# Kernel optimization log

Hardware: AMD Instinct MI355X
Metric: run time of the kernel (lower is better)

## Reference

```python
import jax, jax.numpy as jnp
import numpy as np

B, L, E, H = 4, 2048, 1024, 16
D = E // H
RBF_GAMMA = 0.5


def setup_inputs() -> dict:
    key = jax.random.key(0)
    ks = jax.random.split(key, 8)
    s = 1.0 / np.sqrt(E)  # linear init scale
    return {
        "query": jax.random.normal(ks[0], (B, L, E), jnp.float32),
        "key": jax.random.normal(ks[1], (B, L, E), jnp.float32),
        "value": jax.random.normal(ks[2], (B, L, E), jnp.float32),
        "Wq": jax.random.normal(ks[3], (E, E), jnp.float32) * s,
        "bq": jnp.zeros((E,), jnp.float32),
        "Wk": jax.random.normal(ks[4], (E, E), jnp.float32) * s,
        "bk": jnp.zeros((E,), jnp.float32),
        "Wv": jax.random.normal(ks[5], (E, E), jnp.float32) * s,
        "bv": jnp.zeros((E,), jnp.float32),
        "Wo": jax.random.normal(ks[6], (E, E), jnp.float32) * s,
        "bo": jnp.zeros((E,), jnp.float32),
    }


def _heads(x):
    # (B, L, E) -> (B, H, L, D)
    b, l, _ = x.shape
    return x.reshape(b, l, H, D).transpose(0, 2, 1, 3)


def _rbf_scores(q, k):
    # score[b,h,i,j] = -gamma * ||q_i - k_j||^2   (log of RBF kernel)
    q2 = jnp.sum(q * q, axis=-1)  # (B,H,Lq)
    k2 = jnp.sum(k * k, axis=-1)  # (B,H,Lk)
    qk = jnp.einsum("bhqd,bhkd->bhqk", q, k)  # (B,H,Lq,Lk)
    sqd = q2[..., :, None] + k2[..., None, :] - 2.0 * qk
    return -RBF_GAMMA * sqd


def reference(query, key, value, Wq, bq, Wk, bk, Wv, bv, Wo, bo):
    # Linear projections (torch nn.Linear: x @ W.T + b)
    q = _heads(query @ Wq.T + bq)
    k = _heads(key @ Wk.T + bk)
    v = _heads(value @ Wv.T + bv)
    scores = _rbf_scores(q, k)            # (B,H,L,L)
    attn = jax.nn.softmax(scores, axis=-1)  # dropout p=0.0 (eval)
    out = jnp.einsum("bhqk,bhkd->bhqd", attn, v)
    out = out.transpose(0, 2, 1, 3).reshape(B, L, E)  # merge heads
    return out @ Wo.T + bo
```

## Files before the change

### kernel.cpp

```cpp
#include <hip/hip_runtime.h>
#include <hip/hip_bf16.h>
#include <stdint.h>

#define DEV __device__ __forceinline__

typedef __attribute__((ext_vector_type(8))) __bf16 bf16x8;
typedef __attribute__((ext_vector_type(4))) float f32x4;
typedef __attribute__((ext_vector_type(16))) float f32x16;
typedef __attribute__((ext_vector_type(2))) unsigned int u32x2;
typedef __attribute__((ext_vector_type(4))) unsigned int u32x4;

#define LOG2E 1.44269504088896f

DEV unsigned short f2bf(float f) {
    union { float f; unsigned int u; } v; v.f = f;
    unsigned int u = v.u;
    return (unsigned short)((u + 0x7FFFu + ((u >> 16) & 1u)) >> 16);
}
DEV float bf2f(unsigned short s) {
    union { unsigned int u; float f; } v; v.u = ((unsigned int)s) << 16;
    return v.f;
}

DEV f32x4 mfma16(bf16x8 a, bf16x8 b, f32x4 c) {
    return __builtin_amdgcn_mfma_f32_16x16x32_bf16(a, b, c, 0, 0, 0);
}
DEV f32x16 mfma32(bf16x8 a, bf16x8 b, f32x16 c) {
    return __builtin_amdgcn_mfma_f32_32x32x16_bf16(a, b, c, 0, 0, 0);
}
DEV float exp2a(float x) { float r; asm("v_exp_f32 %0, %1" : "=v"(r) : "v"(x)); return r; }
DEV unsigned cvtpk(float lo, float hi) {
    unsigned r; asm("v_cvt_pk_bf16_f32 %0, %1, %2" : "=v"(r) : "v"(lo), "v"(hi)); return r;
}
DEV void plswap(unsigned& x, unsigned& y) {
    asm volatile("v_permlane32_swap_b32 %0, %1" : "+v"(x), "+v"(y));
}

#define GLOAD_LDS16(g, l)                                                          \
    __builtin_amdgcn_global_load_lds((__attribute__((address_space(1))) void*)(g), \
                                     (__attribute__((address_space(3))) void*)(l), \
                                     16, 0, 0)

#define VMCNT(N) asm volatile("s_waitcnt vmcnt(" #N ")" ::: "memory")
#define LGKM0    asm volatile("s_waitcnt lgkmcnt(0)" ::: "memory")
#define RBAR()   do { __builtin_amdgcn_s_barrier(); __builtin_amdgcn_sched_barrier(0); } while (0)

__global__ void k_cvtw(const float* __restrict__ i0, const float* __restrict__ i1,
                       const float* __restrict__ i2, const float* __restrict__ i3,
                       unsigned short* __restrict__ o0, unsigned short* __restrict__ o1,
                       unsigned short* __restrict__ o2, unsigned short* __restrict__ o3) {
    int z = blockIdx.y;
    const float* in = z == 0 ? i0 : (z == 1 ? i1 : (z == 2 ? i2 : i3));
    unsigned short* out = z == 0 ? o0 : (z == 1 ? o1 : (z == 2 ? o2 : o3));
    float scale = z == 0 ? LOG2E : 1.0f;
    int stride = gridDim.x * blockDim.x;
    for (int i = blockIdx.x * blockDim.x + threadIdx.x; i * 4 < 1048576; i += stride) {
        float4 f = reinterpret_cast<const float4*>(in)[i];
        ushort4 o;
        o.x = f2bf(f.x * scale); o.y = f2bf(f.y * scale);
        o.z = f2bf(f.z * scale); o.w = f2bf(f.w * scale);
        reinterpret_cast<ushort4*>(out)[i] = o;
    }
}

__global__ __launch_bounds__(256) void k_gemm_qkv(
    const float* __restrict__ aq, const float* __restrict__ ak, const float* __restrict__ av,
    const unsigned short* __restrict__ wq, const unsigned short* __restrict__ wk,
    const unsigned short* __restrict__ wv,
    const float* __restrict__ bq, const float* __restrict__ bk, const float* __restrict__ bv,
    unsigned short* __restrict__ Qb, unsigned short* __restrict__ Kb,
    unsigned short* __restrict__ VbT, float* __restrict__ biask) {
    __shared__ __align__(16) unsigned short SMEM[24576];
    unsigned short* As = SMEM;
    unsigned short* Bs = SMEM + 8192;

    const int flat = blockIdx.x;
    const int xcd = flat & 7;
    const int bn = (flat >> 3) & 7;
    const int row = xcd * 24 + (flat >> 6);
    const int z = row >> 6;
    const int bm = row & 63;

    const float* A = z == 0 ? aq : (z == 1 ? ak : av);
    const unsigned short* Bw = z == 0 ? wq : (z == 1 ? wk : wv);
    const float* bias = z == 0 ? bq : (z == 1 ? bk : bv);
    const float bscale = z == 0 ? LOG2E : 1.0f;
    const int K = 1024;

    const int tid = threadIdx.x;
    const int lane = tid & 63, w = tid >> 6;
    const int g = lane >> 4, cc = lane & 15;
    const int wm = w >> 1, wn = w & 1;

    f32x4 acc[4][4] = {};
    const int srow = lane >> 3;
    const int scol = (lane & 7) * 8;

    float4 ar[4][2];
    auto loadA = [&](int kt) {
#pragma unroll
        for (int p = 0; p < 4; ++p) {
            int c = w * 4 + p;
            int rr = c * 8 + srow;
            const float* gA = A + (size_t)(bm * 128 + rr) * K + kt + scol;
            ar[p][0] = *reinterpret_cast<const float4*>(gA);
            ar[p][1] = *reinterpret_cast<const float4*>(gA + 4);
        }
    };
    auto writeA = [&]() {
#pragma unroll
        for (int p = 0; p < 4; ++p) {
            int c = w * 4 + p;
            u32x4 pk;
            pk[0] = cvtpk(ar[p][0].x, ar[p][0].y);
            pk[1] = cvtpk(ar[p][0].z, ar[p][0].w);
            pk[2] = cvtpk(ar[p][1].x, ar[p][1].y);
            pk[3] = cvtpk(ar[p][1].z, ar[p][1].w);
            *reinterpret_cast<u32x4*>(&As[c * 512 + srow * 64 + scol]) = pk;
        }
    };
    auto issueB = [&](int kt, int buf) {
#pragma unroll
        for (int p = 0; p < 4; ++p) {
            int c = w * 4 + p;
            int rr = c * 8 + srow;
            const unsigned short* gB = Bw + (size_t)(bn * 128 + rr) * K + kt + scol;
            GLOAD_LDS16(gB, &Bs[buf * 8192 + c * 512]);
        }
    };
    auto compute = [&](int buf) {
        const unsigned short* Bc = &Bs[buf * 8192];
#pragma unroll
        for (int kc = 0; kc < 2; ++kc) {
            bf16x8 af[4], bf[4];
#pragma unroll
            for (int i = 0; i < 4; ++i) {
                af[i] = *reinterpret_cast<const bf16x8*>(&As[(wm * 64 + i * 16 + cc) * 64 + kc * 32 + g * 8]);
                bf[i] = *reinterpret_cast<const bf16x8*>(&Bc[(wn * 64 + i * 16 + cc) * 64 + kc * 32 + g * 8]);
            }
#pragma unroll
            for (int mi = 0; mi < 4; ++mi)
#pragma unroll
                for (int nj = 0; nj < 4; ++nj)
                    acc[mi][nj] = mfma16(af[mi], bf[nj], acc[mi][nj]);
        }
    };

    loadA(0);
    issueB(0, 0);
    issueB(64, 1);
    VMCNT(8);
    writeA();
    loadA(64);
    VMCNT(12);
    LGKM0; RBAR();
    compute(0);
    RBAR();
    for (int kt = 64; kt < 960; kt += 64) {
        int c = (kt >> 6) & 1;
        issueB(kt + 64, c ^ 1);
        VMCNT(4);
        writeA();
        loadA(kt + 64);
        LGKM0; RBAR();
        compute(c);
        RBAR();
    }
    VMCNT(0);
    writeA();
    LGKM0; RBAR();
    compute(1);

    if (z == 2) {
        __syncthreads();
        unsigned short* T = SMEM;
#pragma unroll
        for (int mi = 0; mi < 4; ++mi) {
#pragma unroll
            for (int nj = 0; nj < 4; ++nj) {
                int nl = wn * 64 + nj * 16 + cc;
                float bvv = bias[bn * 128 + nl];
                int m0 = wm * 64 + mi * 16 + g * 4;
                u32x2 pr;
                pr[0] = cvtpk(acc[mi][nj][0] + bvv, acc[mi][nj][1] + bvv);
                pr[1] = cvtpk(acc[mi][nj][2] + bvv, acc[mi][nj][3] + bvv);
                *reinterpret_cast<u32x2*>(&T[nl * 136 + m0]) = pr;
            }
        }
        __syncthreads();
        const int b = bm >> 4;
        const int l0 = (bm & 15) * 128;
        const int h0 = bn * 2;
#pragma unroll
        for (int p = 0; p < 8; ++p) {
            int n = p * 16 + (tid >> 4);
            int chunk = tid & 15;
            u32x4 v = *reinterpret_cast<const u32x4*>(&T[n * 136 + chunk * 8]);
            int h = h0 + (n >> 6), d = n & 63;
            *reinterpret_cast<u32x4*>(
                &VbT[(((size_t)b * 16 + h) * 64 + d) * 2048 + l0 + chunk * 8]) = v;
        }
        return;
    }

    unsigned short* out = z == 0 ? Qb : Kb;
    float sq[4][4];
#pragma unroll
    for (int mi = 0; mi < 4; ++mi)
#pragma unroll
        for (int r = 0; r < 4; ++r) sq[mi][r] = 0.f;

#pragma unroll
    for (int mi = 0; mi < 4; ++mi) {
#pragma unroll
        for (int nj = 0; nj < 4; ++nj) {
            int n = bn * 128 + wn * 64 + nj * 16 + cc;
            float bvv = bias[n] * bscale;
            int h = n >> 6, d = n & 63;
#pragma unroll
            for (int r = 0; r < 4; ++r) {
                int m = bm * 128 + wm * 64 + mi * 16 + g * 4 + r;
                unsigned short us = f2bf(acc[mi][nj][r] + bvv);
                int b = m >> 11, l = m & 2047;
                out[(((size_t)b * 16 + h) * 2048 + l) * 64 + d] = us;
                if (z == 1) { float vr = bf2f(us); sq[mi][r] += vr * vr; }
            }
        }
    }
    if (z == 1) {
        const int h = bn * 2 + wn;
#pragma unroll
        for (int mi = 0; mi < 4; ++mi)
#pragma unroll
            for (int r = 0; r < 4; ++r) {
                float s = sq[mi][r];
                s += __shfl_xor(s, 1); s += __shfl_xor(s, 2);
                s += __shfl_xor(s, 4); s += __shfl_xor(s, 8);
                if (cc == 0) {
                    int m = bm * 128 + wm * 64 + mi * 16 + g * 4 + r;
                    biask[(((size_t)(m >> 11)) * 16 + h) * 2048 + (m & 2047)] =
                        -0.5f * LOG2E * s;
                }
            }
    }
}

__global__ __launch_bounds__(256) void k_gemm_out(const unsigned short* __restrict__ A,
                                                  const unsigned short* __restrict__ Bw,
                                                  const float* __restrict__ bias,
                                                  float* __restrict__ out) {
    __shared__ __align__(16) unsigned short As[128 * 64];
    __shared__ __align__(16) unsigned short Bs[128 * 64];
    const int K = 1024, N = 1024;
    const int flat = blockIdx.x;
    const int xcd = flat & 7;
    const int bn = (flat >> 3) & 7;
    const int bm = xcd * 8 + (flat >> 6);

    const int tid = threadIdx.x;
    const int lane = tid & 63, w = tid >> 6;
    const int g = lane >> 4, cc = lane & 15;
    const int wm = w >> 1, wn = w & 1;

    f32x4 acc[4][4] = {};
    const int srow = lane >> 3;
    const int scol = (lane & 7) * 8;

    for (int kt = 0; kt < K; kt += 64) {
#pragma unroll
        for (int p = 0; p < 4; ++p) {
            int c = w * 4 + p;
            int rr = c * 8 + srow;
            const unsigned short* gA = A + (size_t)(bm * 128 + rr) * K + kt + scol;
            GLOAD_LDS16(gA, &As[c * 512]);
            const unsigned short* gB = Bw + (size_t)(bn * 128 + rr) * K + kt + scol;
            GLOAD_LDS16(gB, &Bs[c * 512]);
        }
        __syncthreads();
#pragma unroll
        for (int kc = 0; kc < 2; ++kc) {
            bf16x8 af[4], bf[4];
#pragma unroll
            for (int i = 0; i < 4; ++i) {
                af[i] = *reinterpret_cast<const bf16x8*>(&As[(wm * 64 + i * 16 + cc) * 64 + kc * 32 + g * 8]);
                bf[i] = *reinterpret_cast<const bf16x8*>(&Bs[(wn * 64 + i * 16 + cc) * 64 + kc * 32 + g * 8]);
            }
#pragma unroll
            for (int mi = 0; mi < 4; ++mi)
#pragma unroll
                for (int nj = 0; nj < 4; ++nj)
                    acc[mi][nj] = mfma16(af[mi], bf[nj], acc[mi][nj]);
        }
        __syncthreads();
    }

#pragma unroll
    for (int mi = 0; mi < 4; ++mi) {
#pragma unroll
        for (int nj = 0; nj < 4; ++nj) {
            int n = bn * 128 + wn * 64 + nj * 16 + cc;
            float bvv = bias[n];
#pragma unroll
            for (int r = 0; r < 4; ++r) {
                int m = bm * 128 + wm * 64 + mi * 16 + g * 4 + r;
                out[(size_t)m * N + n] = acc[mi][nj][r] + bvv;
            }
        }
    }
}

__global__ __launch_bounds__(256, 2) void k_attn5(const unsigned short* __restrict__ Q,
                                                  const unsigned short* __restrict__ K,
                                                  const unsigned short* __restrict__ VT,
                                                  const float* __restrict__ biask,
                                                  unsigned short* __restrict__ Ob) {
    __shared__ __align__(16) unsigned short SM[18432];
    const int tid = threadIdx.x;
    const int lane = tid & 63, w = tid >> 6;
    const int l31 = lane & 31, hi = lane >> 5, l7 = lane & 7;
    const int flat = blockIdx.x;
    const int bh = (flat & 7) * 8 + ((flat >> 3) & 7);
    const int qt = flat >> 6;
    const size_t kvbase = (size_t)bh * 2048 * 64;
    const int q0 = qt * 256 + w * 64;

    bf16x8 qf[2][4];
#pragma unroll
    for (int qb = 0; qb < 2; ++qb)
#pragma unroll
        for (int kc = 0; kc < 4; ++kc)
            qf[qb][kc] = *reinterpret_cast<const bf16x8*>(
                Q + kvbase + (size_t)(q0 + qb * 32 + l31) * 64 + kc * 16 + hi * 8);

    f32x16 ot[2][2] = {};
    float lrun[2] = {0.f, 0.f};
    const int srow = lane >> 3;

    auto stage = [&](int buf, int t) {
        const int kO = buf ? 4096 : 0;
        const int vO = buf ? 12288 : 8192;
#pragma unroll
        for (int i = 0; i < 2; ++i) {
            int r = w * 16 + i * 8 + srow;
            int cb = l7 ^ (r & 7);
            const unsigned short* gk = K + kvbase + (size_t)(t * 64 + r) * 64 + cb * 8;
            GLOAD_LDS16(gk, &SM[kO + (w * 16 + i * 8) * 64]);
            const unsigned short* gv = VT + kvbase + (size_t)r * 2048 + t * 64 + cb * 8;
            GLOAD_LDS16(gv, &SM[vO + (w * 16 + i * 8) * 64]);
        }
        if (w == 0 && lane < 16) {
            const float* gb = biask + bh * 2048 + t * 64 + lane * 4;
            GLOAD_LDS16(gb, &SM[buf ? 16512 : 16384]);
        }
    };

    stage(0, 0);
    int cur = 0;
    for (int t = 0; t < 32; ++t) {
        __syncthreads();
        if (t + 1 < 32) stage(cur ^ 1, t + 1);
        const int kO = cur ? 4096 : 0;
        const int vO = cur ? 12288 : 8192;
        const float* Bl = reinterpret_cast<const float*>(&SM[cur ? 16512 : 16384]);

        f32x4 bb[2][4];
#pragma unroll
        for (int t2 = 0; t2 < 2; ++t2)
#pragma unroll
            for (int g2 = 0; g2 < 4; ++g2)
                bb[t2][g2] = *reinterpret_cast<const f32x4*>(Bl + t2 * 32 + g2 * 8 + hi * 4);

        f32x16 st[2][2];
#pragma unroll
        for (int qb = 0; qb < 2; ++qb)
#pragma unroll
            for (int t2 = 0; t2 < 2; ++t2)
#pragma unroll
                for (int g2 = 0; g2 < 4; ++g2)
#pragma unroll
                    for (int j = 0; j < 4; ++j) st[qb][t2][g2 * 4 + j] = bb[t2][g2][j];

        __builtin_amdgcn_s_setprio(1);
#pragma unroll
        for (int kc = 0; kc < 4; ++kc)
#pragma unroll
            for (int t2 = 0; t2 < 2; ++t2) {
                bf16x8 kf = *reinterpret_cast<const bf16x8*>(
                    &SM[kO + (t2 * 32 + l31) * 64 + ((((kc << 1) | hi) ^ l7) << 3)]);
                st[0][t2] = mfma32(kf, qf[0][kc], st[0][t2]);
                st[1][t2] = mfma32(kf, qf[1][kc], st[1][t2]);
            }
        __builtin_amdgcn_s_setprio(0);

#pragma unroll
        for (int qb = 0; qb < 2; ++qb) {
            float r0 = 0.f, r1 = 0.f;
#pragma unroll
            for (int i = 0; i < 16; ++i) {
                float p0 = exp2a(st[qb][0][i]); st[qb][0][i] = p0; r0 += p0;
                float p1 = exp2a(st[qb][1][i]); st[qb][1][i] = p1; r1 += p1;
            }
            lrun[qb] += r0 + r1;
        }

#pragma unroll
        for (int t2 = 0; t2 < 2; ++t2) {
            bf16x8 fA[2], fB[2];
#pragma unroll
            for (int qb = 0; qb < 2; ++qb) {
                unsigned w0 = cvtpk(st[qb][t2][0], st[qb][t2][1]);
                unsigned w1 = cvtpk(st[qb][t2][2], st[qb][t2][3]);
                unsigned w2 = cvtpk(st[qb][t2][4], st[qb][t2][5]);
                unsigned w3 = cvtpk(st[qb][t2][6], st[qb][t2][7]);
                unsigned w4 = cvtpk(st[qb][t2][8], st[qb][t2][9]);
                unsigned w5 = cvtpk(st[qb][t2][10], st[qb][t2][11]);
                unsigned w6 = cvtpk(st[qb][t2][12], st[qb][t2][13]);
                unsigned w7 = cvtpk(st[qb][t2][14], st[qb][t2][15]);
                plswap(w0, w2); plswap(w1, w3); plswap(w4, w6); plswap(w5, w7);
                u32x4 p0, p1;
                p0[0] = w0; p0[1] = w1; p0[2] = w2; p0[3] = w3;
                p1[0] = w4; p1[1] = w5; p1[2] = w6; p1[3] = w7;
                fA[qb] = __builtin_bit_cast(bf16x8, p0);
                fB[qb] = __builtin_bit_cast(bf16x8, p1);
            }
            const int kb0 = t2 * 2, kb1 = t2 * 2 + 1;
            __builtin_amdgcn_s_setprio(1);
#pragma unroll
            for (int dj = 0; dj < 2; ++dj) {
                bf16x8 v0 = *reinterpret_cast<const bf16x8*>(
                    &SM[vO + (dj * 32 + l31) * 64 + ((((kb0 << 1) | hi) ^ l7) << 3)]);
                bf16x8 v1 = *reinterpret_cast<const bf16x8*>(
                    &SM[vO + (dj * 32 + l31) * 64 + ((((kb1 << 1) | hi) ^ l7) << 3)]);
                ot[0][dj] = mfma32(v0, fA[0], ot[0][dj]);
                ot[0][dj] = mfma32(v1, fB[0], ot[0][dj]);
                ot[1][dj] = mfma32(v0, fA[1], ot[1][dj]);
                ot[1][dj] = mfma32(v1, fB[1], ot[1][dj]);
            }
            __builtin_amdgcn_s_setprio(0);
        }
        cur ^= 1;
    }

    lrun[0] += __shfl_xor(lrun[0], 32);
    lrun[1] += __shfl_xor(lrun[1], 32);

    __syncthreads();
#pragma unroll
    for (int qb = 0; qb < 2; ++qb) {
        float inv = 1.0f / lrun[qb];
        const int base = (w * 64 + qb * 32 + l31) * 72;
#pragma unroll
        for (int dj = 0; dj < 2; ++dj)
#pragma unroll
            for (int i = 0; i < 8; ++i) {
                unsigned pr = cvtpk(ot[qb][dj][2 * i] * inv, ot[qb][dj][2 * i + 1] * inv);
                int d0 = dj * 32 + 2 * (i & 1) + 8 * (i >> 1) + 4 * hi;
                *reinterpret_cast<unsigned*>(&SM[base + d0]) = pr;
            }
    }
    __syncthreads();
    const int b = bh >> 4, h = bh & 15;
#pragma unroll
    for (int pass = 0; pass < 8; ++pass) {
        int row = pass * 32 + (tid >> 3);
        int seg = tid & 7;
        u32x4 vdat = *reinterpret_cast<const u32x4*>(&SM[row * 72 + seg * 8]);
        int l = qt * 256 + row;
        *reinterpret_cast<u32x4*>(Ob + ((size_t)b * 2048 + l) * 1024 + h * 64 + seg * 8) = vdat;
    }
}

extern "C" void kernel_launch(void* const* d_in, const int* in_sizes, int n_in,
                              void* d_out, int out_size, void* d_ws, size_t ws_size,
                              hipStream_t stream) {
    const float* query = (const float*)d_in[0];
    const float* key   = (const float*)d_in[1];
    const float* value = (const float*)d_in[2];
    const float* Wq = (const float*)d_in[3];
    const float* bq = (const float*)d_in[4];
    const float* Wk = (const float*)d_in[5];
    const float* bk = (const float*)d_in[6];
    const float* Wv = (const float*)d_in[7];
    const float* bv = (const float*)d_in[8];
    const float* Wo = (const float*)d_in[9];
    const float* bo = (const float*)d_in[10];

    unsigned short* VbT = (unsigned short*)d_ws;
    unsigned short* wq = VbT + 8388608;
    unsigned short* wk = wq + 1048576;
    unsigned short* wv = wk + 1048576;
    unsigned short* wo = wv + 1048576;
    unsigned short* Qb = wo + 1048576;
    unsigned short* Kb = Qb + 8388608;
    unsigned short* Ob = Kb + 8388608;
    float* biask = (float*)(Ob + 8388608);

    k_cvtw<<<dim3(256, 4), 256, 0, stream>>>(Wq, Wk, Wv, Wo, wq, wk, wv, wo);

    k_gemm_qkv<<<1536, 256, 0, stream>>>(query, key, value, wq, wk, wv,
                                         bq, bk, bv, Qb, Kb, VbT, biask);

    k_attn5<<<512, 256, 0, stream>>>(Qb, Kb, VbT, biask, Ob);

    k_gemm_out<<<512, 256, 0, stream>>>(Ob, wo, bo, (float*)d_out);
}
```

Baseline: 198.0 us.

## Double-buffer output GEMM LDS loads and raise wave priority during MFMA

The output projection GEMM now keeps two LDS stages and prefetches tile k+2 while computing tile k, waiting on vmcnt instead of a full barrier after each load. This is meant to hide global-to-LDS latency behind MFMA work. It also wraps the MFMA compute sections of both GEMMs in s_setprio to favor waves issuing matrix ops. LDS use doubles to 64KB per block, which may reduce occupancy.

```diff
diff --git a/kernel.cpp b/kernel.cpp
--- a/kernel.cpp
+++ b/kernel.cpp
@@ -130,6 +130,7 @@
     };
     auto compute = [&](int buf) {
         const unsigned short* Bc = &Bs[buf * 8192];
+        __builtin_amdgcn_s_setprio(1);
 #pragma unroll
         for (int kc = 0; kc < 2; ++kc) {
             bf16x8 af[4], bf[4];
@@ -144,6 +145,7 @@
                 for (int nj = 0; nj < 4; ++nj)
                     acc[mi][nj] = mfma16(af[mi], bf[nj], acc[mi][nj]);
         }
+        __builtin_amdgcn_s_setprio(0);
     };
 
     loadA(0);
@@ -249,8 +251,7 @@
                                                   const unsigned short* __restrict__ Bw,
                                                   const float* __restrict__ bias,
                                                   float* __restrict__ out) {
-    __shared__ __align__(16) unsigned short As[128 * 64];
-    __shared__ __align__(16) unsigned short Bs[128 * 64];
+    __shared__ __align__(16) unsigned short SMEM[32768];
     const int K = 1024, N = 1024;
     const int flat = blockIdx.x;
     const int xcd = flat & 7;
@@ -266,24 +267,28 @@
     const int srow = lane >> 3;
     const int scol = (lane & 7) * 8;
 
-    for (int kt = 0; kt < K; kt += 64) {
+    auto stage = [&](int kt, int buf) {
+        unsigned short* SB = &SMEM[buf * 16384];
 #pragma unroll
         for (int p = 0; p < 4; ++p) {
             int c = w * 4 + p;
             int rr = c * 8 + srow;
             const unsigned short* gA = A + (size_t)(bm * 128 + rr) * K + kt + scol;
-            GLOAD_LDS16(gA, &As[c * 512]);
+            GLOAD_LDS16(gA, &SB[c * 512]);
             const unsigned short* gB = Bw + (size_t)(bn * 128 + rr) * K + kt + scol;
-            GLOAD_LDS16(gB, &Bs[c * 512]);
-        }
-        __syncthreads();
+            GLOAD_LDS16(gB, &SB[8192 + c * 512]);
+        }
+    };
+    auto compute = [&](int buf) {
+        const unsigned short* SB = &SMEM[buf * 16384];
+        __builtin_amdgcn_s_setprio(1);
 #pragma unroll
         for (int kc = 0; kc < 2; ++kc) {
             bf16x8 af[4], bf[4];
 #pragma unroll
             for (int i = 0; i < 4; ++i) {
-                af[i] = *reinterpret_cast<const bf16x8*>(&As[(wm * 64 + i * 16 + cc) * 64 + kc * 32 + g * 8]);
-                bf[i] = *reinterpret_cast<const bf16x8*>(&Bs[(wn * 64 + i * 16 + cc) * 64 + kc * 32 + g * 8]);
+                af[i] = *reinterpret_cast<const bf16x8*>(&SB[(wm * 64 + i * 16 + cc) * 64 + kc * 32 + g * 8]);
+                bf[i] = *reinterpret_cast<const bf16x8*>(&SB[8192 + (wn * 64 + i * 16 + cc) * 64 + kc * 32 + g * 8]);
             }
 #pragma unroll
             for (int mi = 0; mi < 4; ++mi)
@@ -291,8 +296,22 @@
                 for (int nj = 0; nj < 4; ++nj)
                     acc[mi][nj] = mfma16(af[mi], bf[nj], acc[mi][nj]);
         }
-        __syncthreads();
-    }
+        __builtin_amdgcn_s_setprio(0);
+    };
+
+    stage(0, 0);
+    stage(64, 1);
+    for (int kt = 0; kt < 960; kt += 64) {
+        int c = (kt >> 6) & 1;
+        VMCNT(8);
+        RBAR();
+        compute(c);
+        RBAR();
+        if (kt + 128 < K) stage(kt + 128, c);
+    }
+    VMCNT(0);
+    RBAR();
+    compute(1);
 
 #pragma unroll
     for (int mi = 0; mi < 4; ++mi) {
```

After: 192.2 us, median of 2. 1.03x faster.
